# Optimization experiments

Measured on AMD Instinct MI355X. Metric: run time of the kernel, lower is better.

Reference implementation:

```python
import jax, jax.numpy as jnp
import numpy as np

B, N, G = 32, 262144, 256


def setup_inputs() -> dict:
    key = jax.random.key(0)
    k1, k2, k3 = jax.random.split(key, 3)
    pr = jax.random.normal(k1, (B, N), dtype=jnp.float32)
    inp_means = jax.random.normal(k2, (B, G), dtype=jnp.float32)
    vr = jax.random.randint(k3, (B, N, 1), 0, G, dtype=jnp.int32)
    W = jnp.ones((2,), dtype=jnp.float32)  # hist_weight, ones initializer
    return {"pr": pr, "inp_means": inp_means, "vr": vr, "W": W}


def reference(pr, inp_means, vr, W):
    sg = jax.lax.stop_gradient
    G = inp_means.shape[1]
    v = jnp.squeeze(vr, -1)  # [B, N] int cluster ids (stop_gradient in orig; int anyway)
    p_sg = sg(pr)

    # Per-batch segmented min/max/sum/any over clusters (replaces python loop over g).
    def seg(p, psg, vi):
        mn = jnp.full((G,), jnp.inf, p.dtype).at[vi].min(psg)    # min(where(gidx, pr, inf))
        mx = jnp.full((G,), -jnp.inf, p.dtype).at[vi].max(psg)   # max(where(gidx, pr, -inf))
        sm = jnp.zeros((G,), p.dtype).at[vi].add(p)              # sum(where(gidx, pr, 0))
        any_ = jnp.zeros((G,), bool).at[vi].set(True)            # reduce_any(gidx)
        return mn, mx, sm, any_

    vmins, vmaxs, vsum, vany = jax.vmap(seg)(pr, p_sg, v)  # each [B, G]
    # Original divides sum by cast(any)->1.0 (or 0/0=nan -> 0), i.e. the group SUM.
    vmeans = jnp.where(vany, vsum, jnp.zeros((), pr.dtype))
    vmeans = (inp_means * W[0] + vmeans * W[1]) / (W[0] + W[1])

    no_scale = vmins == vmaxs  # [B, G]
    vmins_g = jnp.take_along_axis(jnp.where(no_scale, 0.0, vmins), v, axis=1)  # [B, N]
    vmaxs_g = jnp.take_along_axis(jnp.where(no_scale, 1.0, vmaxs), v, axis=1)  # [B, N]

    sort_ids = jnp.argsort(vmeans, axis=1)
    orig_ids = jnp.argsort(sort_ids, axis=1)  # inverse permutation
    vs = jnp.take_along_axis(vmeans, sort_ids, axis=1)  # [B, G]
    cd = jnp.concatenate([vs[:, :1], vs, vs[:, -1:] * 2], axis=1)  # [B, G+2]
    # conv1d with kernel ones(2)/c, VALID: out[i] = (cd[i] + cd[i+1]) / c
    f0 = (cd[:, :-2] + cd[:, 1:-1]) / 1.999  # conv(...)[:, :-1]
    f1 = (cd[:, 1:-1] + cd[:, 2:]) / 2.001   # conv(...)[:, 1:]
    f0 = jnp.take_along_axis(
        jnp.where(no_scale, 0.0, jnp.take_along_axis(f0, orig_ids, axis=1)), v, axis=1)
    f1 = jnp.take_along_axis(
        jnp.where(no_scale, 1.0, jnp.take_along_axis(f1, orig_ids, axis=1)), v, axis=1)

    tmp = (sg(pr) - sg(vmins_g)) / sg(vmaxs_g - vmins_g) * (f1 - f0) + f0  # [B, N]
    bad = jnp.isnan(tmp) | (tmp == 0.0)
    s = pr / jnp.where(bad, 1.0, tmp)  # safe denominator (grad-safe)
    scale = jnp.where(bad | jnp.isnan(s) | jnp.isinf(s), 0.0, s)
    return pr * scale
```

## Files before the change

kernel.cpp:

```cpp
#include <hip/hip_runtime.h>
#include <math.h>

#define NB 32
#define NN 262144
#define NG 256
#define NC 128
#define CH (NN/NC)
#define SC (CH/4)
#define CD 64
#define ELD (NN/CD)

__global__ __launch_bounds__(256, 8) void k_count(const int* __restrict__ vr,
                                                  unsigned long long* __restrict__ wcnt16,
                                                  unsigned short* __restrict__ cnt16,
                                                  unsigned* __restrict__ gid32){
  __shared__ unsigned sc[4][NG];
  const int t    = threadIdx.x;
  const int lane = t & 63;
  const int w    = t >> 6;
  sc[0][t] = 0u; sc[1][t] = 0u; sc[2][t] = 0u; sc[3][t] = 0u;
  __syncthreads();

  const int b = blockIdx.x / NC;
  const int c = blockIdx.x % NC;
  const size_t base = (size_t)b*NN + (size_t)c*CH;
  const int4* v4 = (const int4*)(vr + base);

#pragma unroll
  for (int i = 0; i < 2; i++){
    int idx = w*128 + i*64 + lane;
    int4 v = v4[idx];
    atomicAdd(&sc[w][v.x], 1u);
    atomicAdd(&sc[w][v.y], 1u);
    atomicAdd(&sc[w][v.z], 1u);
    atomicAdd(&sc[w][v.w], 1u);
    gid32[(base >> 2) + idx] =
      (unsigned)v.x | ((unsigned)v.y << 8) | ((unsigned)v.z << 16) | ((unsigned)v.w << 24);
  }
  __syncthreads();

  unsigned c0 = sc[0][t], c1 = sc[1][t], c2 = sc[2][t], c3 = sc[3][t];
  const size_t cb = (size_t)b*NC + c;
  wcnt16[cb*NG + t] = (unsigned long long)c0
                    | ((unsigned long long)c1 << 16)
                    | ((unsigned long long)c2 << 32)
                    | ((unsigned long long)c3 << 48);
  cnt16[cb*NG + t] = (unsigned short)(c0 + c1 + c2 + c3);
}

__global__ __launch_bounds__(256, 8) void k_scatter(const float* __restrict__ pr,
                                                    const unsigned* __restrict__ gid32,
                                                    const unsigned long long* __restrict__ wcnt16,
                                                    const unsigned short* __restrict__ cnt16,
                                                    float* __restrict__ sorted,
                                                    unsigned* __restrict__ grpbase,
                                                    unsigned* __restrict__ grplen){
  __shared__ float vbuf[CH];
  __shared__ unsigned char gbuf[CH];
  __shared__ unsigned wcnt[4][NG];
  __shared__ unsigned bias[NG];
  __shared__ unsigned wsumA[4];
  __shared__ unsigned wsumO[4];
  const int t    = threadIdx.x;
  const int lane = t & 63;
  const int w    = t >> 6;
  const int b = blockIdx.x / NC;
  const int c = blockIdx.x % NC;
  const size_t base = (size_t)b*NN + (size_t)c*CH;

  {
    const unsigned short* colT = cnt16 + (size_t)b*NC*NG + t;
    unsigned tot_all = 0, tot_before = 0;
#pragma unroll 8
    for (int cc = 0; cc < NC; cc++){
      unsigned tt = colT[(size_t)cc*NG];
      tot_all += tt;
      if (cc < c) tot_before += tt;
    }
    unsigned long long own = wcnt16[((size_t)b*NC + c)*NG + t];
    unsigned lo = (unsigned)own, hi = (unsigned)(own >> 32);
    unsigned w0 = lo & 0xFFFFu, w1 = lo >> 16, w2 = hi & 0xFFFFu, w3 = hi >> 16;
    unsigned tot_own = w0 + w1 + w2 + w3;

    unsigned va = tot_all, vo = tot_own;
#pragma unroll
    for (int d = 1; d < 64; d <<= 1){
      unsigned ya = __shfl_up(va, d, 64);
      unsigned yo = __shfl_up(vo, d, 64);
      if (lane >= d){ va += ya; vo += yo; }
    }
    if (lane == 63){ wsumA[w] = va; wsumO[w] = vo; }
    __syncthreads();
    unsigned preA = 0, preO = 0;
#pragma unroll
    for (int k = 0; k < 3; k++) if (k < w){ preA += wsumA[k]; preO += wsumO[k]; }
    unsigned base_g = preA + va - tot_all;
    unsigned lb     = preO + vo - tot_own;
    wcnt[0][t] = lb;
    wcnt[1][t] = lb + w0;
    wcnt[2][t] = lb + w0 + w1;
    wcnt[3][t] = lb + w0 + w1 + w2;
    bias[t] = (base_g + tot_before) - lb;
    if (c == 0){
      grpbase[b*NG + t] = base_g;
      grplen [b*NG + t] = tot_all;
    }
  }
  __syncthreads();

  {
    const float*    psrc = pr    + base        + (size_t)w*SC;
    const unsigned* gsrc = gid32 + (base >> 2) + (size_t)w*(SC/4);
    const int shft = (lane & 3) * 8;

    float pv[8]; unsigned pk[8];
#pragma unroll
    for (int s = 0; s < 8; s++){
      pv[s] = psrc[s*64 + lane];
      pk[s] = gsrc[s*16 + (lane >> 2)];
    }
#pragma unroll
    for (int s = 0; s < 8; s++){
      int g = (int)((pk[s] >> shft) & 255u);
      unsigned slot = atomicAdd(&wcnt[w][g], 1u);
      vbuf[slot] = pv[s];
      gbuf[slot] = (unsigned char)g;
    }
  }
  __syncthreads();

  {
    float* dst = sorted + (size_t)b*NN;
    const unsigned* gbuf32 = (const unsigned*)gbuf;
#pragma unroll
    for (int k = 0; k < CH/256; k++){
      int p = k*256 + t;
      unsigned packed = gbuf32[p >> 2];
      unsigned g = (packed >> ((p & 3) * 8)) & 255u;
      dst[bias[g] + (unsigned)p] = vbuf[p];
    }
  }
}

__global__ __launch_bounds__(32) void k_sum(const float* __restrict__ sorted,
                                            const unsigned* __restrict__ grpbase,
                                            const unsigned* __restrict__ grplen,
                                            float* __restrict__ gsum,
                                            float* __restrict__ gmn,
                                            float* __restrict__ gmx){
  const int lane = threadIdx.x;
  const int b = blockIdx.x >> 3;
  const int g = ((blockIdx.x & 7) << 5) + lane;

  const unsigned base = grpbase[b*NG + g];
  const unsigned len  = grplen [b*NG + g];
  const float* sp = sorted + (size_t)b*NN + base;

  float s = 0.0f, mn = INFINITY, mx = -INFINITY;

  unsigned head = (4u - ((unsigned)(((size_t)sp) >> 2) & 3u)) & 3u;
  if (head > len) head = len;
  for (unsigned i = 0; i < head; i++){
    float v = sp[i];
    s = __fadd_rn(s, v); mn = fminf(mn, v); mx = fmaxf(mx, v);
  }
  const float4* f4 = (const float4*)(sp + head);
  const unsigned rem   = len - head;
  const unsigned nfull = rem >> 4;

  float4 b0[4], b1[4], b2[4], b3[4], b4[4], b5[4], b6[4], b7[4];
#define LOADV(D, K) { D[0]=f4[(K)*4+0]; D[1]=f4[(K)*4+1]; D[2]=f4[(K)*4+2]; D[3]=f4[(K)*4+3]; }
#define CONS1(V)    { s=__fadd_rn(s,(V)); mn=fminf(mn,(V)); mx=fmaxf(mx,(V)); }
#define CONSV(D)    { _Pragma("unroll") for (int j = 0; j < 4; j++){ float4 q = D[j]; \
                      CONS1(q.x) CONS1(q.y) CONS1(q.z) CONS1(q.w) } }

  if (nfull > 0) LOADV(b0, 0)
  if (nfull > 1) LOADV(b1, 1)
  if (nfull > 2) LOADV(b2, 2)
  if (nfull > 3) LOADV(b3, 3)
  if (nfull > 4) LOADV(b4, 4)
  if (nfull > 5) LOADV(b5, 5)
  if (nfull > 6) LOADV(b6, 6)
  if (nfull > 7) LOADV(b7, 7)
  unsigned k = 0;
  for (; k + 8 <= nfull; k += 8){
    CONSV(b0) if (k +  8 < nfull) LOADV(b0, k +  8)
    CONSV(b1) if (k +  9 < nfull) LOADV(b1, k +  9)
    CONSV(b2) if (k + 10 < nfull) LOADV(b2, k + 10)
    CONSV(b3) if (k + 11 < nfull) LOADV(b3, k + 11)
    CONSV(b4) if (k + 12 < nfull) LOADV(b4, k + 12)
    CONSV(b5) if (k + 13 < nfull) LOADV(b5, k + 13)
    CONSV(b6) if (k + 14 < nfull) LOADV(b6, k + 14)
    CONSV(b7) if (k + 15 < nfull) LOADV(b7, k + 15)
  }
  {
    unsigned r = nfull - k;
    if (r > 0) CONSV(b0)
    if (r > 1) CONSV(b1)
    if (r > 2) CONSV(b2)
    if (r > 3) CONSV(b3)
    if (r > 4) CONSV(b4)
    if (r > 5) CONSV(b5)
    if (r > 6) CONSV(b6)
  }
  for (unsigned i = head + (nfull << 4); i < len; i++){
    float v = sp[i];
    s = __fadd_rn(s, v); mn = fminf(mn, v); mx = fmaxf(mx, v);
  }
#undef LOADV
#undef CONS1
#undef CONSV

  gsum[b*NG + g] = s;
  gmn [b*NG + g] = mn;
  gmx [b*NG + g] = mx;
}

__global__ __launch_bounds__(256) void k_pipeline(const float* __restrict__ gsum,
                                                  const float* __restrict__ gmn,
                                                  const float* __restrict__ gmx,
                                                  const float* __restrict__ inp_means,
                                                  const float* __restrict__ Wv,
                                                  float* __restrict__ params){
  const int b = blockIdx.x;
  const int g = threadIdx.x;
  __shared__ float vm[NG];
  __shared__ float vs[NG];

  const float s   = gsum[b*NG + g];
  const float mnf = gmn [b*NG + g];
  const float mxf = gmx [b*NG + g];
  const float W0 = Wv[0], W1 = Wv[1];
  float mean = __fdiv_rn(__fadd_rn(__fmul_rn(inp_means[b*NG + g], W0),
                                   __fmul_rn(s, W1)),
                         __fadd_rn(W0, W1));
  vm[g] = mean;
  __syncthreads();

  int r = 0;
  for (int j = 0; j < NG; j++){
    float x = vm[j];
    r += (x < mean) || (x == mean && j < g);
  }
  vs[r] = mean;
  __syncthreads();

  float c0 = (r == 0)    ? vs[0]                     : vs[r-1];
  float c1 = vs[r];
  float c2 = (r == NG-1) ? __fmul_rn(vs[NG-1], 2.0f) : vs[r+1];
  float f0 = __fdiv_rn(__fadd_rn(c0, c1), 1.999f);
  float f1 = __fdiv_rn(__fadd_rn(c1, c2), 2.001f);

  bool ns = (mnf == mxf);
  params[(b*4 + 0)*NG + g] = ns ? 0.0f : mnf;
  params[(b*4 + 1)*NG + g] = ns ? 1.0f : __fsub_rn(mxf, mnf);
  params[(b*4 + 2)*NG + g] = ns ? 1.0f : __fsub_rn(f1, f0);
  params[(b*4 + 3)*NG + g] = ns ? 0.0f : f0;
}

static __device__ __forceinline__ float apply_one(float p, unsigned g,
                                                  const float* __restrict__ sp0,
                                                  const float* __restrict__ sp1,
                                                  const float* __restrict__ sp2,
                                                  const float* __restrict__ sp3){
  float t1  = __fsub_rn(p, sp0[g]);
  float t3  = __fdiv_rn(t1, sp1[g]);
  float t5  = __fmul_rn(t3, sp2[g]);
  float tmp = __fadd_rn(t5, sp3[g]);
  bool bad = __builtin_isnan(tmp) || (tmp == 0.0f);
  float s = __fdiv_rn(p, bad ? 1.0f : tmp);
  bool bad2 = bad || __builtin_isnan(s) || __builtin_isinf(s);
  float sc = bad2 ? 0.0f : s;
  return __fmul_rn(p, sc);
}

__global__ __launch_bounds__(256) void k_apply(const float* __restrict__ pr,
                                               const unsigned* __restrict__ gid32,
                                               const float* __restrict__ params,
                                               float* __restrict__ out){
  __shared__ float sp0[NG], sp1[NG], sp2[NG], sp3[NG];
  const int t = threadIdx.x;
  const int b = blockIdx.x / CD;
  const int c = blockIdx.x % CD;

  sp0[t] = params[(b*4 + 0)*NG + t];
  sp1[t] = params[(b*4 + 1)*NG + t];
  sp2[t] = params[(b*4 + 2)*NG + t];
  sp3[t] = params[(b*4 + 3)*NG + t];
  __syncthreads();

  const size_t base = (size_t)b*NN + (size_t)c*ELD;
  const float4* p4 = (const float4*)(pr + base);
  float4* o4 = (float4*)(out + base);

#pragma unroll
  for (int i = 0; i < ELD/1024; i++){
    float4 p = p4[i*256 + t];
    unsigned pk = gid32[(base >> 2) + i*256 + t];
    float4 r;
    r.x = apply_one(p.x,  pk        & 255u, sp0, sp1, sp2, sp3);
    r.y = apply_one(p.y, (pk >>  8) & 255u, sp0, sp1, sp2, sp3);
    r.z = apply_one(p.z, (pk >> 16) & 255u, sp0, sp1, sp2, sp3);
    r.w = apply_one(p.w,  pk >> 24,         sp0, sp1, sp2, sp3);
    o4[i*256 + t] = r;
  }
}

extern "C" void kernel_launch(void* const* d_in, const int* in_sizes, int n_in,
                              void* d_out, int out_size, void* d_ws, size_t ws_size,
                              hipStream_t stream){
  const float* pr        = (const float*)d_in[0];
  const float* inp_means = (const float*)d_in[1];
  const int*   vr        = (const int*)d_in[2];
  const float* W         = (const float*)d_in[3];
  float* out = (float*)d_out;

  char* ws = (char*)d_ws;
  size_t o = 0;
  unsigned long long* wcnt16 = (unsigned long long*)(ws + o); o += (size_t)NB*NC*NG*8;
  unsigned short* cnt16 = (unsigned short*)(ws + o); o += (size_t)NB*NC*NG*2;
  unsigned* gid32   = (unsigned*)(ws + o); o += (size_t)NB*NN;
  unsigned* grpbase = (unsigned*)(ws + o); o += (size_t)NB*NG*4;
  unsigned* grplen  = (unsigned*)(ws + o); o += (size_t)NB*NG*4;
  float*    gsum    = (float*)   (ws + o); o += (size_t)NB*NG*4;
  float*    gmn     = (float*)   (ws + o); o += (size_t)NB*NG*4;
  float*    gmx     = (float*)   (ws + o); o += (size_t)NB*NG*4;
  float*    params  = (float*)   (ws + o); o += (size_t)NB*NG*16;
  float* sorted = out;

  k_count   <<<NB*NC, 256, 0, stream>>>(vr, wcnt16, cnt16, gid32);
  k_scatter <<<NB*NC, 256, 0, stream>>>(pr, gid32, wcnt16, cnt16, sorted, grpbase, grplen);
  k_sum     <<<NB*8,   32, 0, stream>>>(sorted, grpbase, grplen, gsum, gmn, gmx);
  k_pipeline<<<NB,    256, 0, stream>>>(gsum, gmn, gmx, inp_means, W, params);
  k_apply   <<<NB*CD, 256, 0, stream>>>(pr, gid32, params, out);
}
```

Before: 181.6 us.

## Double chunk size and use eight sub-histograms with 512-thread scatter blocks

Halves the number of chunks per batch, so each block handles twice as many elements. Counting now keeps eight per-wave local histograms packed into 128-bit records, and the scatter kernel runs 512 threads with eight waves. The goal is to shorten the column prefix scan over chunk counts and to cut block count and per-block overhead. In exchange, each block uses more shared memory (about 24KB of buffers) and there are fewer blocks, which may lower occupancy.

```diff
diff --git a/kernel.cpp b/kernel.cpp
--- a/kernel.cpp
+++ b/kernel.cpp
@@ -4,21 +4,23 @@
 #define NB 32
 #define NN 262144
 #define NG 256
-#define NC 128
+#define NC 64
 #define CH (NN/NC)
-#define SC (CH/4)
+#define NW 8
+#define SW (CH/NW)
 #define CD 64
 #define ELD (NN/CD)
 
-__global__ __launch_bounds__(256, 8) void k_count(const int* __restrict__ vr,
-                                                  unsigned long long* __restrict__ wcnt16,
-                                                  unsigned short* __restrict__ cnt16,
-                                                  unsigned* __restrict__ gid32){
-  __shared__ unsigned sc[4][NG];
+__global__ __launch_bounds__(256) void k_count(const int* __restrict__ vr,
+                                               ulonglong2* __restrict__ wcnt16,
+                                               unsigned short* __restrict__ cnt16,
+                                               unsigned* __restrict__ gid32){
+  __shared__ unsigned sc[NW][NG];
   const int t    = threadIdx.x;
   const int lane = t & 63;
   const int w    = t >> 6;
-  sc[0][t] = 0u; sc[1][t] = 0u; sc[2][t] = 0u; sc[3][t] = 0u;
+#pragma unroll
+  for (int k = 0; k < NW; k++) sc[k][t] = 0u;
   __syncthreads();
 
   const int b = blockIdx.x / NC;
@@ -27,37 +29,41 @@
   const int4* v4 = (const int4*)(vr + base);
 
 #pragma unroll
-  for (int i = 0; i < 2; i++){
-    int idx = w*128 + i*64 + lane;
+  for (int i = 0; i < 4; i++){
+    int idx = w*256 + i*64 + lane;
+    int sw  = 2*w + (i >> 1);
     int4 v = v4[idx];
-    atomicAdd(&sc[w][v.x], 1u);
-    atomicAdd(&sc[w][v.y], 1u);
-    atomicAdd(&sc[w][v.z], 1u);
-    atomicAdd(&sc[w][v.w], 1u);
+    atomicAdd(&sc[sw][v.x], 1u);
+    atomicAdd(&sc[sw][v.y], 1u);
+    atomicAdd(&sc[sw][v.z], 1u);
+    atomicAdd(&sc[sw][v.w], 1u);
     gid32[(base >> 2) + idx] =
       (unsigned)v.x | ((unsigned)v.y << 8) | ((unsigned)v.z << 16) | ((unsigned)v.w << 24);
   }
   __syncthreads();
 
-  unsigned c0 = sc[0][t], c1 = sc[1][t], c2 = sc[2][t], c3 = sc[3][t];
+  unsigned s0 = sc[0][t], s1 = sc[1][t], s2 = sc[2][t], s3 = sc[3][t];
+  unsigned s4 = sc[4][t], s5 = sc[5][t], s6 = sc[6][t], s7 = sc[7][t];
   const size_t cb = (size_t)b*NC + c;
-  wcnt16[cb*NG + t] = (unsigned long long)c0
-                    | ((unsigned long long)c1 << 16)
-                    | ((unsigned long long)c2 << 32)
-                    | ((unsigned long long)c3 << 48);
-  cnt16[cb*NG + t] = (unsigned short)(c0 + c1 + c2 + c3);
-}
-
-__global__ __launch_bounds__(256, 8) void k_scatter(const float* __restrict__ pr,
-                                                    const unsigned* __restrict__ gid32,
-                                                    const unsigned long long* __restrict__ wcnt16,
-                                                    const unsigned short* __restrict__ cnt16,
-                                                    float* __restrict__ sorted,
-                                                    unsigned* __restrict__ grpbase,
-                                                    unsigned* __restrict__ grplen){
+  ulonglong2 r;
+  r.x = (unsigned long long)s0 | ((unsigned long long)s1 << 16)
+      | ((unsigned long long)s2 << 32) | ((unsigned long long)s3 << 48);
+  r.y = (unsigned long long)s4 | ((unsigned long long)s5 << 16)
+      | ((unsigned long long)s6 << 32) | ((unsigned long long)s7 << 48);
+  wcnt16[cb*NG + t] = r;
+  cnt16 [cb*NG + t] = (unsigned short)(s0+s1+s2+s3+s4+s5+s6+s7);
+}
+
+__global__ __launch_bounds__(512) void k_scatter(const float* __restrict__ pr,
+                                                 const unsigned* __restrict__ gid32,
+                                                 const ulonglong2* __restrict__ wcnt16,
+                                                 const unsigned short* __restrict__ cnt16,
+                                                 float* __restrict__ sorted,
+                                                 unsigned* __restrict__ grpbase,
+                                                 unsigned* __restrict__ grplen){
   __shared__ float vbuf[CH];
   __shared__ unsigned char gbuf[CH];
-  __shared__ unsigned wcnt[4][NG];
+  __shared__ unsigned wcnt[NW][NG];
   __shared__ unsigned bias[NG];
   __shared__ unsigned wsumA[4];
   __shared__ unsigned wsumO[4];
@@ -68,21 +74,25 @@
   const int c = blockIdx.x % NC;
   const size_t base = (size_t)b*NN + (size_t)c*CH;
 
-  {
+  unsigned s0=0,s1=0,s2=0,s3=0,s4=0,s5=0,s6=0,s7=0;
+  unsigned tot_all=0, tot_before=0, tot_own=0, va=0, vo=0;
+  if (t < NG){
     const unsigned short* colT = cnt16 + (size_t)b*NC*NG + t;
-    unsigned tot_all = 0, tot_before = 0;
 #pragma unroll 8
     for (int cc = 0; cc < NC; cc++){
       unsigned tt = colT[(size_t)cc*NG];
       tot_all += tt;
       if (cc < c) tot_before += tt;
     }
-    unsigned long long own = wcnt16[((size_t)b*NC + c)*NG + t];
-    unsigned lo = (unsigned)own, hi = (unsigned)(own >> 32);
-    unsigned w0 = lo & 0xFFFFu, w1 = lo >> 16, w2 = hi & 0xFFFFu, w3 = hi >> 16;
-    unsigned tot_own = w0 + w1 + w2 + w3;
-
-    unsigned va = tot_all, vo = tot_own;
+    ulonglong2 own = wcnt16[((size_t)b*NC + c)*NG + t];
+    unsigned long long lo = own.x, hi = own.y;
+    s0 = (unsigned)(lo & 0xFFFF); s1 = (unsigned)((lo >> 16) & 0xFFFF);
+    s2 = (unsigned)((lo >> 32) & 0xFFFF); s3 = (unsigned)(lo >> 48);
+    s4 = (unsigned)(hi & 0xFFFF); s5 = (unsigned)((hi >> 16) & 0xFFFF);
+    s6 = (unsigned)((hi >> 32) & 0xFFFF); s7 = (unsigned)(hi >> 48);
+    tot_own = s0+s1+s2+s3+s4+s5+s6+s7;
+
+    va = tot_all; vo = tot_own;
 #pragma unroll
     for (int d = 1; d < 64; d <<= 1){
       unsigned ya = __shfl_up(va, d, 64);
@@ -90,16 +100,23 @@
       if (lane >= d){ va += ya; vo += yo; }
     }
     if (lane == 63){ wsumA[w] = va; wsumO[w] = vo; }
-    __syncthreads();
+  }
+  __syncthreads();
+  if (t < NG){
     unsigned preA = 0, preO = 0;
 #pragma unroll
     for (int k = 0; k < 3; k++) if (k < w){ preA += wsumA[k]; preO += wsumO[k]; }
     unsigned base_g = preA + va - tot_all;
     unsigned lb     = preO + vo - tot_own;
-    wcnt[0][t] = lb;
-    wcnt[1][t] = lb + w0;
-    wcnt[2][t] = lb + w0 + w1;
-    wcnt[3][t] = lb + w0 + w1 + w2;
+    unsigned r = lb;
+    wcnt[0][t] = r; r += s0;
+    wcnt[1][t] = r; r += s1;
+    wcnt[2][t] = r; r += s2;
+    wcnt[3][t] = r; r += s3;
+    wcnt[4][t] = r; r += s4;
+    wcnt[5][t] = r; r += s5;
+    wcnt[6][t] = r; r += s6;
+    wcnt[7][t] = r;
     bias[t] = (base_g + tot_before) - lb;
     if (c == 0){
       grpbase[b*NG + t] = base_g;
@@ -109,8 +126,8 @@
   __syncthreads();
 
   {
-    const float*    psrc = pr    + base        + (size_t)w*SC;
-    const unsigned* gsrc = gid32 + (base >> 2) + (size_t)w*(SC/4);
+    const float*    psrc = pr    + base        + (size_t)w*SW;
+    const unsigned* gsrc = gid32 + (base >> 2) + (size_t)w*(SW/4);
     const int shft = (lane & 3) * 8;
 
     float pv[8]; unsigned pk[8];
@@ -133,8 +150,8 @@
     float* dst = sorted + (size_t)b*NN;
     const unsigned* gbuf32 = (const unsigned*)gbuf;
 #pragma unroll
-    for (int k = 0; k < CH/256; k++){
-      int p = k*256 + t;
+    for (int k = 0; k < CH/512; k++){
+      int p = k*512 + t;
       unsigned packed = gbuf32[p >> 2];
       unsigned g = (packed >> ((p & 3) * 8)) & 255u;
       dst[bias[g] + (unsigned)p] = vbuf[p];
@@ -317,7 +334,7 @@
 
   char* ws = (char*)d_ws;
   size_t o = 0;
-  unsigned long long* wcnt16 = (unsigned long long*)(ws + o); o += (size_t)NB*NC*NG*8;
+  ulonglong2* wcnt16 = (ulonglong2*)(ws + o); o += (size_t)NB*NC*NG*16;
   unsigned short* cnt16 = (unsigned short*)(ws + o); o += (size_t)NB*NC*NG*2;
   unsigned* gid32   = (unsigned*)(ws + o); o += (size_t)NB*NN;
   unsigned* grpbase = (unsigned*)(ws + o); o += (size_t)NB*NG*4;
@@ -329,7 +346,7 @@
   float* sorted = out;
 
   k_count   <<<NB*NC, 256, 0, stream>>>(vr, wcnt16, cnt16, gid32);
-  k_scatter <<<NB*NC, 256, 0, stream>>>(pr, gid32, wcnt16, cnt16, sorted, grpbase, grplen);
+  k_scatter <<<NB*NC, 512, 0, stream>>>(pr, gid32, wcnt16, cnt16, sorted, grpbase, grplen);
   k_sum     <<<NB*8,   32, 0, stream>>>(sorted, grpbase, grplen, gsum, gmn, gmx);
   k_pipeline<<<NB,    256, 0, stream>>>(gsum, gmn, gmx, inp_means, W, params);
   k_apply   <<<NB*CD, 256, 0, stream>>>(pr, gid32, params, out);
```

Result: faster. 160.7 us, median of 2 (-11.5%).
